# Optimization experiments

Hardware: AMD Instinct MI355X
Metric: run time of the kernel (lower is better)

## Reference

```python
import jax, jax.numpy as jnp
import numpy as np

T, A = 2048, 64          # n_thread, n_agents
RAWOB, N_TP, N_GP = 120, 5, 2
E = N_TP * N_GP          # number of sub-nets (type x group placeholder)
D = RAWOB + N_TP + 1     # augmented obs dim fed to each Net
H = 128                  # hidden width of each sub-net MLP
N_ACTION = 16


def setup_inputs() -> dict:
    key = jax.random.key(0)
    ks = jax.random.split(key, 12)
    s1 = 1.0 / np.sqrt(D)
    s2 = 1.0 / np.sqrt(H)
    return {
        "obs": jax.random.normal(ks[0], (T, A, RAWOB), dtype=jnp.float32),
        "hete_pick": jax.random.randint(ks[1], (T, A), 0, E),
        "hete_type": jax.random.randint(ks[2], (T, A), 0, N_TP),
        "gp_sel_summary": jax.random.randint(ks[3], (T, N_TP), 0, N_GP),
        # per-expert actor MLP params [E, ...]
        "W1": jax.random.normal(ks[4], (E, D, H), dtype=jnp.float32) * s1,
        "b1": jnp.zeros((E, H), dtype=jnp.float32),
        "W2": jax.random.normal(ks[5], (E, H, N_ACTION), dtype=jnp.float32) * s2,
        "b2": jnp.zeros((E, N_ACTION), dtype=jnp.float32),
        # central critic params
        "Wc1": jax.random.normal(ks[6], (D, H), dtype=jnp.float32) * s1,
        "bc1": jnp.zeros((H,), dtype=jnp.float32),
        "Wc2": jax.random.normal(ks[7], (H, 1), dtype=jnp.float32) * s2,
        "bc2": jnp.zeros((1,), dtype=jnp.float32),
    }


def _augment_obs(obs, hete_type, gp_sel_summary):
    # obs <- cat(obs, hete_type, gp_sel_summary with -1 scattered at own type idx)
    t, a, _ = obs.shape
    n_tp = gp_sel_summary.shape[1]
    gp = jnp.broadcast_to(gp_sel_summary[:, None, :].astype(obs.dtype), (t, a, n_tp))
    oh = jax.nn.one_hot(hete_type, n_tp, dtype=obs.dtype)
    gp_obs = gp * (1.0 - oh) - oh  # scatter -1 at index hete_type
    return jnp.concatenate([obs, hete_type[..., None].astype(obs.dtype), gp_obs], axis=-1)


def reference(obs, hete_pick, hete_type, gp_sel_summary,
              W1, b1, W2, b2, Wc1, bc1, Wc2, bc2):
    t, a, _ = obs.shape
    x = _augment_obs(obs, hete_type, gp_sel_summary)          # [T, A, D]
    xf = x.reshape(t * a, -1)                                  # [N, D]
    pick = hete_pick.reshape(t * a)                            # [N]
    n_exp = W1.shape[0]
    # dispatch: each token routed to exactly one sub-net; dense compute + masked combine
    logits = jnp.zeros((t * a, W2.shape[-1]), dtype=obs.dtype)
    for e in range(n_exp):  # small fixed expert loop
        y = jax.nn.relu(xf @ W1[e] + b1[e]) @ W2[e] + b2[e]    # [N, n_action]
        logits = jnp.where((pick == e)[:, None], y, logits)
    logits = logits.reshape(t, a, -1)
    # central critic on all tokens
    value = (jax.nn.relu(xf @ Wc1 + bc1) @ Wc2 + bc2).reshape(t, a, 1)
    return logits, value
```

## Files before the change

kernel.cpp:

```cpp
#include <hip/hip_runtime.h>
#include <hip/hip_bf16.h>

#define T_DIM   2048
#define A_DIM   64
#define N_TOK   (T_DIM * A_DIM)
#define RAWOB   120
#define N_TP    5
#define E_EXP   10
#define D_DIM   126
#define DP      128
#define H_DIM   128
#define N_ACT   16
#define CAP     16384
#define MTILE   64
#define MAXC    (CAP / MTILE)
#define LOGITS_SZ (N_TOK * N_ACT)
#define XS_STRIDE 136

typedef __bf16 bh8 __attribute__((ext_vector_type(8)));
typedef float  f32x4 __attribute__((ext_vector_type(4)));

__device__ __forceinline__ f32x4 mfma16(bh8 a, bh8 b, f32x4 c) {
    return __builtin_amdgcn_mfma_f32_16x16x32_bf16(a, b, c, 0, 0, 0);
}

__device__ __forceinline__ float bf2f(ushort u) {
    unsigned x = ((unsigned)u) << 16;
    return __builtin_bit_cast(float, x);
}
__device__ __forceinline__ ushort f2bf(float f) {
    unsigned x = __builtin_bit_cast(unsigned, f);
    unsigned r = (x + 0x7fffu + ((x >> 16) & 1u)) >> 16;
    return (ushort)r;
}

#define W1T_N (E_EXP * H_DIM * DP)
#define W2T_N (E_EXP * N_ACT * H_DIM)
#define WC1T_N (DP * DP)
#define PREP_BLOCKS 124

__global__ __launch_bounds__(256) void prep_kernel(
    const float* __restrict__ W1, const float* __restrict__ W2,
    const float* __restrict__ Wc1,
    int* __restrict__ counts, ushort* __restrict__ W1t,
    ushort* __restrict__ W2t, ushort* __restrict__ Wc1t)
{
    int bx = blockIdx.x, tid = threadIdx.x;
    if (bx < 44) {
        __shared__ ushort st[32][130];
        const float* src;
        ushort* dstbase;
        int d0;
        if (bx < 40) {
            int e = bx >> 2;
            d0 = (bx & 3) * 32;
            src = W1 + (e * D_DIM + d0) * H_DIM;
            dstbase = W1t + e * H_DIM * DP;
        } else {
            d0 = (bx - 40) * 32;
            src = Wc1 + d0 * H_DIM;
            dstbase = Wc1t;
        }
        int dmax = D_DIM - d0;
#pragma unroll
        for (int p = 0; p < 16; ++p) {
            int idx = p * 256 + tid;
            int dd = idx >> 7, h = idx & 127;
            float v = (dd < dmax) ? src[dd * H_DIM + h] : 0.f;
            st[dd][h] = f2bf(v);
        }
        __syncthreads();
#pragma unroll
        for (int p = 0; p < 16; ++p) {
            int idx = p * 256 + tid;
            int h = idx >> 5, d = idx & 31;
            dstbase[h * DP + d0 + d] = st[d][h];
        }
    } else {
        int i = (bx - 44) * 256 + tid;
        int h = i & 127;
        int a = (i >> 7) & 15;
        int e = i >> 11;
        W2t[(e * N_ACT + a) * H_DIM + h] = f2bf(W2[(e * H_DIM + h) * N_ACT + a]);
        if (bx == 44 && tid < 160) counts[tid] = 0;
    }
}

#define BUCKET_BLOCKS 128
__global__ __launch_bounds__(256) void bucket_kernel(
    const int* __restrict__ pick, int* __restrict__ counts, int* __restrict__ order)
{
    __shared__ int lc[E_EXP], lb[E_EXP], lcur[E_EXP];
    int tid = threadIdx.x;
    if (tid < E_EXP) { lc[tid] = 0; lcur[tid] = 0; }
    __syncthreads();
    int base = blockIdx.x * 1024;
    int e4[4];
#pragma unroll
    for (int it = 0; it < 4; ++it) {
        e4[it] = pick[base + it * 256 + tid];
        atomicAdd(&lc[e4[it]], 1);
    }
    __syncthreads();
    if (tid < E_EXP) lb[tid] = atomicAdd(&counts[tid * 16], lc[tid]);
    __syncthreads();
#pragma unroll
    for (int it = 0; it < 4; ++it) {
        int e = e4[it];
        int pos = lb[e] + atomicAdd(&lcur[e], 1);
        if (pos < CAP) order[e * CAP + pos] = base + it * 256 + tid;
    }
}

__device__ __forceinline__ void gemm64_relu(
    const ushort* xs, const ushort* __restrict__ Wt,
    const float* __restrict__ bias, ushort* hs, int w, int l)
{
    const int n0 = w * 32;
    const int lm = l & 15;
    const int lq = l >> 4;

    f32x4 acc[4][2];
#pragma unroll
    for (int mt = 0; mt < 4; ++mt) {
        acc[mt][0] = (f32x4){0.f, 0.f, 0.f, 0.f};
        acc[mt][1] = (f32x4){0.f, 0.f, 0.f, 0.f};
    }
    bh8 bfrag[4][2];
#pragma unroll
    for (int kt = 0; kt < 4; ++kt)
#pragma unroll
        for (int nt = 0; nt < 2; ++nt)
            bfrag[kt][nt] = *(const bh8*)(const void*)
                (Wt + (n0 + nt * 16 + lm) * DP + kt * 32 + lq * 8);

#pragma unroll
    for (int kt = 0; kt < 4; ++kt) {
#pragma unroll
        for (int mt = 0; mt < 4; ++mt) {
            bh8 a = *(const bh8*)(const void*)
                (xs + (mt * 16 + lm) * XS_STRIDE + kt * 32 + lq * 8);
            acc[mt][0] = mfma16(a, bfrag[kt][0], acc[mt][0]);
            acc[mt][1] = mfma16(a, bfrag[kt][1], acc[mt][1]);
        }
    }
    float bn0 = bias[n0 + lm];
    float bn1 = bias[n0 + 16 + lm];
#pragma unroll
    for (int mt = 0; mt < 4; ++mt) {
#pragma unroll
        for (int nt = 0; nt < 2; ++nt) {
            float bn = nt ? bn1 : bn0;
            int n = n0 + nt * 16 + lm;
#pragma unroll
            for (int r = 0; r < 4; ++r) {
                int m = mt * 16 + lq * 4 + r;
                float vf = acc[mt][nt][r] + bn;
                vf = fmaxf(vf, 0.f);
                hs[m * XS_STRIDE + n] = f2bf(vf);
            }
        }
    }
}

__global__ __launch_bounds__(256) void moe_kernel(
    const float* __restrict__ obs, const int* __restrict__ hete_type,
    const int* __restrict__ gp_sel,
    const float* __restrict__ b1, const float* __restrict__ b2,
    const float* __restrict__ bc1, const float* __restrict__ bc2,
    const int* __restrict__ counts, const int* __restrict__ order,
    const ushort* __restrict__ W1t, const ushort* __restrict__ W2t,
    const ushort* __restrict__ Wc1t, const float* __restrict__ Wc2,
    float* __restrict__ out)
{
    __shared__ int idx_s[MTILE];
    __shared__ __align__(16) ushort xs[MTILE * XS_STRIDE];
    __shared__ __align__(16) ushort hs[MTILE * XS_STRIDE];
    __shared__ float wc2s[128];

    const int bx = blockIdx.x;
    const int e = bx % E_EXP;
    const int c = bx / E_EXP;
    const int cnt = counts[e * 16];
    const int start = c * MTILE;
    if (start >= cnt) return;
    const int v = min(MTILE, cnt - start);

    const int tid = threadIdx.x;
    if (tid < MTILE) {
        int tok = 0;
        if (tid < v) tok = order[e * CAP + start + tid];
        idx_s[tid] = tok;
    } else if (tid < MTILE + 128) {
        wc2s[tid - MTILE] = Wc2[tid - MTILE];
    }
    __syncthreads();

    const int ck = (tid & 15) * 8;
    const int r0 = tid >> 4;
#pragma unroll
    for (int j = 0; j < 4; ++j) {
        int row = r0 + j * 16;
        int tok = idx_s[row];
        ushort* dst = &xs[row * XS_STRIDE + ck];
        if (ck < RAWOB) {
            const float* src = obs + tok * RAWOB + ck;
            float4 u0 = *(const float4*)(const void*)src;
            float4 u1 = *(const float4*)(const void*)(src + 4);
            dst[0] = f2bf(u0.x); dst[1] = f2bf(u0.y);
            dst[2] = f2bf(u0.z); dst[3] = f2bf(u0.w);
            dst[4] = f2bf(u1.x); dst[5] = f2bf(u1.y);
            dst[6] = f2bf(u1.z); dst[7] = f2bf(u1.w);
        } else {
            int ht = hete_type[tok];
            int tt = tok >> 6;
            dst[0] = f2bf((float)ht);
#pragma unroll
            for (int q = 0; q < N_TP; ++q) {
                float g = (q == ht) ? -1.0f : (float)gp_sel[tt * N_TP + q];
                dst[1 + q] = f2bf(g);
            }
            dst[6] = 0; dst[7] = 0;
        }
    }
    __syncthreads();

    const int w = tid >> 6;
    const int l = tid & 63;
    const int lm = l & 15;
    const int lq = l >> 4;

    gemm64_relu(xs, W1t + e * DP * DP, b1 + e * H_DIM, hs, w, l);
    __syncthreads();

    {
        f32x4 acc2 = (f32x4){0.f, 0.f, 0.f, 0.f};
        bh8 bfrag[4];
#pragma unroll
        for (int kt = 0; kt < 4; ++kt)
            bfrag[kt] = *(const bh8*)(const void*)
                (W2t + (e * N_ACT + lm) * H_DIM + kt * 32 + lq * 8);
#pragma unroll
        for (int kt = 0; kt < 4; ++kt) {
            bh8 a = *(const bh8*)(const void*)
                (hs + (w * 16 + lm) * XS_STRIDE + kt * 32 + lq * 8);
            acc2 = mfma16(a, bfrag[kt], acc2);
        }
        float bb = b2[e * N_ACT + lm];
#pragma unroll
        for (int r = 0; r < 4; ++r) {
            int m = w * 16 + lq * 4 + r;
            if (m < v) {
                int tok = idx_s[m];
                out[tok * N_ACT + lm] = acc2[r] + bb;
            }
        }
    }
    __syncthreads();

    gemm64_relu(xs, Wc1t, bc1, hs, w, l);
    __syncthreads();

    if (tid < 128) {
        int m = tid >> 1;
        int half = tid & 1;
        const ushort* hr = &hs[m * XS_STRIDE + half * 64];
        const float* wr = &wc2s[half * 64];
        float s = 0.f;
#pragma unroll
        for (int n = 0; n < 64; ++n) s += bf2f(hr[n]) * wr[n];
        float so = __shfl_xor(s, 1, 64);
        float vt = s + so + bc2[0];
        if (half == 0 && m < v) {
            out[LOGITS_SZ + idx_s[m]] = vt;
        }
    }
}

extern "C" void kernel_launch(void* const* d_in, const int* in_sizes, int n_in,
                              void* d_out, int out_size, void* d_ws, size_t ws_size,
                              hipStream_t stream) {
    const float* obs  = (const float*)d_in[0];
    const int*   pick = (const int*)d_in[1];
    const int*   htyp = (const int*)d_in[2];
    const int*   gp   = (const int*)d_in[3];
    const float* W1   = (const float*)d_in[4];
    const float* b1   = (const float*)d_in[5];
    const float* W2   = (const float*)d_in[6];
    const float* b2   = (const float*)d_in[7];
    const float* Wc1  = (const float*)d_in[8];
    const float* bc1  = (const float*)d_in[9];
    const float* Wc2  = (const float*)d_in[10];
    const float* bc2  = (const float*)d_in[11];
    float* out = (float*)d_out;

    int*    counts = (int*)d_ws;
    int*    order  = counts + 160;
    ushort* W1t    = (ushort*)(order + E_EXP * CAP);
    ushort* W2t    = W1t + W1T_N;
    ushort* Wc1t   = W2t + W2T_N;

    prep_kernel<<<PREP_BLOCKS, 256, 0, stream>>>(
        W1, W2, Wc1, counts, W1t, W2t, Wc1t);
    bucket_kernel<<<BUCKET_BLOCKS, 256, 0, stream>>>(pick, counts, order);
    moe_kernel<<<E_EXP * MAXC, 256, 0, stream>>>(
        obs, htyp, gp, b1, b2, bc1, bc2, counts, order,
        W1t, W2t, Wc1t, Wc2, out);
}
```

Baseline: 158.0 us.

## Halve token tile, fuse critic second layer into registers, raise occupancy

Shrinks the per-block token tile from 64 to 32 rows, which doubles the block count and halves shared memory per block, and adds a launch-bounds occupancy hint of 8 blocks. The critic's second layer (dot with Wc2) is now done in registers via shuffle reductions and a small cross-wave reduction buffer, instead of writing the hidden activations to shared memory and reading them back. This drops one barrier and the hs round trip. In exchange, weight fragments are reloaded per block more often, and only two waves do the actor output GEMM. The per-expert capacity constant is also reduced.

Measured after the change: 160.5 us. About the same (+1.6%).

```diff
diff --git a/kernel.cpp b/kernel.cpp
--- a/kernel.cpp
+++ b/kernel.cpp
@@ -11,8 +11,8 @@
 #define DP      128
 #define H_DIM   128
 #define N_ACT   16
-#define CAP     16384
-#define MTILE   64
+#define CAP     14336
+#define MTILE   32
 #define MAXC    (CAP / MTILE)
 #define LOGITS_SZ (N_TOK * N_ACT)
 #define XS_STRIDE 136
@@ -24,10 +24,6 @@
     return __builtin_amdgcn_mfma_f32_16x16x32_bf16(a, b, c, 0, 0, 0);
 }
 
-__device__ __forceinline__ float bf2f(ushort u) {
-    unsigned x = ((unsigned)u) << 16;
-    return __builtin_bit_cast(float, x);
-}
 __device__ __forceinline__ ushort f2bf(float f) {
     unsigned x = __builtin_bit_cast(unsigned, f);
     unsigned r = (x + 0x7fffu + ((x >> 16) & 1u)) >> 16;
@@ -112,58 +108,7 @@
     }
 }
 
-__device__ __forceinline__ void gemm64_relu(
-    const ushort* xs, const ushort* __restrict__ Wt,
-    const float* __restrict__ bias, ushort* hs, int w, int l)
-{
-    const int n0 = w * 32;
-    const int lm = l & 15;
-    const int lq = l >> 4;
-
-    f32x4 acc[4][2];
-#pragma unroll
-    for (int mt = 0; mt < 4; ++mt) {
-        acc[mt][0] = (f32x4){0.f, 0.f, 0.f, 0.f};
-        acc[mt][1] = (f32x4){0.f, 0.f, 0.f, 0.f};
-    }
-    bh8 bfrag[4][2];
-#pragma unroll
-    for (int kt = 0; kt < 4; ++kt)
-#pragma unroll
-        for (int nt = 0; nt < 2; ++nt)
-            bfrag[kt][nt] = *(const bh8*)(const void*)
-                (Wt + (n0 + nt * 16 + lm) * DP + kt * 32 + lq * 8);
-
-#pragma unroll
-    for (int kt = 0; kt < 4; ++kt) {
-#pragma unroll
-        for (int mt = 0; mt < 4; ++mt) {
-            bh8 a = *(const bh8*)(const void*)
-                (xs + (mt * 16 + lm) * XS_STRIDE + kt * 32 + lq * 8);
-            acc[mt][0] = mfma16(a, bfrag[kt][0], acc[mt][0]);
-            acc[mt][1] = mfma16(a, bfrag[kt][1], acc[mt][1]);
-        }
-    }
-    float bn0 = bias[n0 + lm];
-    float bn1 = bias[n0 + 16 + lm];
-#pragma unroll
-    for (int mt = 0; mt < 4; ++mt) {
-#pragma unroll
-        for (int nt = 0; nt < 2; ++nt) {
-            float bn = nt ? bn1 : bn0;
-            int n = n0 + nt * 16 + lm;
-#pragma unroll
-            for (int r = 0; r < 4; ++r) {
-                int m = mt * 16 + lq * 4 + r;
-                float vf = acc[mt][nt][r] + bn;
-                vf = fmaxf(vf, 0.f);
-                hs[m * XS_STRIDE + n] = f2bf(vf);
-            }
-        }
-    }
-}
-
-__global__ __launch_bounds__(256) void moe_kernel(
+__global__ __launch_bounds__(256, 8) void moe_kernel(
     const float* __restrict__ obs, const int* __restrict__ hete_type,
     const int* __restrict__ gp_sel,
     const float* __restrict__ b1, const float* __restrict__ b2,
@@ -176,7 +121,7 @@
     __shared__ int idx_s[MTILE];
     __shared__ __align__(16) ushort xs[MTILE * XS_STRIDE];
     __shared__ __align__(16) ushort hs[MTILE * XS_STRIDE];
-    __shared__ float wc2s[128];
+    __shared__ float red[4][MTILE];
 
     const int bx = blockIdx.x;
     const int e = bx % E_EXP;
@@ -191,15 +136,13 @@
         int tok = 0;
         if (tid < v) tok = order[e * CAP + start + tid];
         idx_s[tid] = tok;
-    } else if (tid < MTILE + 128) {
-        wc2s[tid - MTILE] = Wc2[tid - MTILE];
     }
     __syncthreads();
 
     const int ck = (tid & 15) * 8;
     const int r0 = tid >> 4;
 #pragma unroll
-    for (int j = 0; j < 4; ++j) {
+    for (int j = 0; j < 2; ++j) {
         int row = r0 + j * 16;
         int tok = idx_s[row];
         ushort* dst = &xs[row * XS_STRIDE + ck];
@@ -229,22 +172,55 @@
     const int l = tid & 63;
     const int lm = l & 15;
     const int lq = l >> 4;
-
-    gemm64_relu(xs, W1t + e * DP * DP, b1 + e * H_DIM, hs, w, l);
-    __syncthreads();
+    const int n0 = w * 32;
 
     {
+        const ushort* Wt = W1t + e * DP * DP;
+        f32x4 acc[2][2];
+#pragma unroll
+        for (int mt = 0; mt < 2; ++mt) {
+            acc[mt][0] = (f32x4){0.f, 0.f, 0.f, 0.f};
+            acc[mt][1] = (f32x4){0.f, 0.f, 0.f, 0.f};
+        }
+#pragma unroll
+        for (int kt = 0; kt < 4; ++kt) {
+            bh8 bf0 = *(const bh8*)(const void*)(Wt + (n0 + lm) * DP + kt * 32 + lq * 8);
+            bh8 bf1 = *(const bh8*)(const void*)(Wt + (n0 + 16 + lm) * DP + kt * 32 + lq * 8);
+#pragma unroll
+            for (int mt = 0; mt < 2; ++mt) {
+                bh8 a = *(const bh8*)(const void*)
+                    (xs + (mt * 16 + lm) * XS_STRIDE + kt * 32 + lq * 8);
+                acc[mt][0] = mfma16(a, bf0, acc[mt][0]);
+                acc[mt][1] = mfma16(a, bf1, acc[mt][1]);
+            }
+        }
+        float bn0 = b1[e * H_DIM + n0 + lm];
+        float bn1 = b1[e * H_DIM + n0 + 16 + lm];
+#pragma unroll
+        for (int mt = 0; mt < 2; ++mt)
+#pragma unroll
+            for (int nt = 0; nt < 2; ++nt) {
+                float bn = nt ? bn1 : bn0;
+                int n = n0 + nt * 16 + lm;
+#pragma unroll
+                for (int r = 0; r < 4; ++r) {
+                    int m = mt * 16 + lq * 4 + r;
+                    float vf = fmaxf(acc[mt][nt][r] + bn, 0.f);
+                    hs[m * XS_STRIDE + n] = f2bf(vf);
+                }
+            }
+    }
+    __syncthreads();
+
+    if (w < 2) {
         f32x4 acc2 = (f32x4){0.f, 0.f, 0.f, 0.f};
-        bh8 bfrag[4];
-#pragma unroll
-        for (int kt = 0; kt < 4; ++kt)
-            bfrag[kt] = *(const bh8*)(const void*)
+#pragma unroll
+        for (int kt = 0; kt < 4; ++kt) {
+            bh8 bf = *(const bh8*)(const void*)
                 (W2t + (e * N_ACT + lm) * H_DIM + kt * 32 + lq * 8);
-#pragma unroll
-        for (int kt = 0; kt < 4; ++kt) {
             bh8 a = *(const bh8*)(const void*)
                 (hs + (w * 16 + lm) * XS_STRIDE + kt * 32 + lq * 8);
-            acc2 = mfma16(a, bfrag[kt], acc2);
+            acc2 = mfma16(a, bf, acc2);
         }
         float bb = b2[e * N_ACT + lm];
 #pragma unroll
@@ -256,24 +232,55 @@
             }
         }
     }
-    __syncthreads();
-
-    gemm64_relu(xs, Wc1t, bc1, hs, w, l);
-    __syncthreads();
-
-    if (tid < 128) {
-        int m = tid >> 1;
-        int half = tid & 1;
-        const ushort* hr = &hs[m * XS_STRIDE + half * 64];
-        const float* wr = &wc2s[half * 64];
-        float s = 0.f;
-#pragma unroll
-        for (int n = 0; n < 64; ++n) s += bf2f(hr[n]) * wr[n];
-        float so = __shfl_xor(s, 1, 64);
-        float vt = s + so + bc2[0];
-        if (half == 0 && m < v) {
-            out[LOGITS_SZ + idx_s[m]] = vt;
-        }
+
+    {
+        f32x4 acc[2][2];
+#pragma unroll
+        for (int mt = 0; mt < 2; ++mt) {
+            acc[mt][0] = (f32x4){0.f, 0.f, 0.f, 0.f};
+            acc[mt][1] = (f32x4){0.f, 0.f, 0.f, 0.f};
+        }
+#pragma unroll
+        for (int kt = 0; kt < 4; ++kt) {
+            bh8 bf0 = *(const bh8*)(const void*)(Wc1t + (n0 + lm) * DP + kt * 32 + lq * 8);
+            bh8 bf1 = *(const bh8*)(const void*)(Wc1t + (n0 + 16 + lm) * DP + kt * 32 + lq * 8);
+#pragma unroll
+            for (int mt = 0; mt < 2; ++mt) {
+                bh8 a = *(const bh8*)(const void*)
+                    (xs + (mt * 16 + lm) * XS_STRIDE + kt * 32 + lq * 8);
+                acc[mt][0] = mfma16(a, bf0, acc[mt][0]);
+                acc[mt][1] = mfma16(a, bf1, acc[mt][1]);
+            }
+        }
+        float bn0 = bc1[n0 + lm],   wcv0 = Wc2[n0 + lm];
+        float bn1 = bc1[n0 + 16 + lm], wcv1 = Wc2[n0 + 16 + lm];
+        float part[2][4];
+#pragma unroll
+        for (int mt = 0; mt < 2; ++mt)
+#pragma unroll
+            for (int r = 0; r < 4; ++r)
+                part[mt][r] = fmaxf(acc[mt][0][r] + bn0, 0.f) * wcv0
+                            + fmaxf(acc[mt][1][r] + bn1, 0.f) * wcv1;
+#pragma unroll
+        for (int mask = 1; mask < 16; mask <<= 1)
+#pragma unroll
+            for (int mt = 0; mt < 2; ++mt)
+#pragma unroll
+                for (int r = 0; r < 4; ++r)
+                    part[mt][r] += __shfl_xor(part[mt][r], mask, 64);
+        if (lm == 0) {
+#pragma unroll
+            for (int mt = 0; mt < 2; ++mt)
+#pragma unroll
+                for (int r = 0; r < 4; ++r)
+                    red[w][mt * 16 + lq * 4 + r] = part[mt][r];
+        }
+    }
+    __syncthreads();
+
+    if (tid < MTILE && tid < v) {
+        float vt = red[0][tid] + red[1][tid] + red[2][tid] + red[3][tid] + bc2[0];
+        out[LOGITS_SZ + idx_s[tid]] = vt;
     }
 }
 
```

## Restructure MoE kernel so each wave owns 16 tokens with register-resident A fragments

Applied to the files above, without the earlier changes.

Each wave now gathers its own 16 tokens straight from global memory into MFMA A-fragments in registers, instead of the whole block staging a 64-row shared tile. The expert and critic first-layer GEMMs are fused into one loop that shares the A fragments. The critic head is reduced in registers with shuffles, which removes its shared-memory pass and all block-level barriers. Each wave now streams the full W1/Wc1 B operands from global/L2 itself rather than splitting N across waves, so weight traffic per token rises. CAP is lowered, occupancy is hinted via launch bounds, and shared memory shrinks to a per-wave hidden buffer.

Result: slower. 192.0 us (+21.6%).

```diff
diff --git a/kernel.cpp b/kernel.cpp
--- a/kernel.cpp
+++ b/kernel.cpp
@@ -11,23 +11,20 @@
 #define DP      128
 #define H_DIM   128
 #define N_ACT   16
-#define CAP     16384
+#define CAP     14336
 #define MTILE   64
 #define MAXC    (CAP / MTILE)
 #define LOGITS_SZ (N_TOK * N_ACT)
-#define XS_STRIDE 136
+#define HB_STRIDE 136
 
 typedef __bf16 bh8 __attribute__((ext_vector_type(8)));
+typedef ushort u16x8 __attribute__((ext_vector_type(8)));
 typedef float  f32x4 __attribute__((ext_vector_type(4)));
 
 __device__ __forceinline__ f32x4 mfma16(bh8 a, bh8 b, f32x4 c) {
     return __builtin_amdgcn_mfma_f32_16x16x32_bf16(a, b, c, 0, 0, 0);
 }
 
-__device__ __forceinline__ float bf2f(ushort u) {
-    unsigned x = ((unsigned)u) << 16;
-    return __builtin_bit_cast(float, x);
-}
 __device__ __forceinline__ ushort f2bf(float f) {
     unsigned x = __builtin_bit_cast(unsigned, f);
     unsigned r = (x + 0x7fffu + ((x >> 16) & 1u)) >> 16;
@@ -112,58 +109,7 @@
     }
 }
 
-__device__ __forceinline__ void gemm64_relu(
-    const ushort* xs, const ushort* __restrict__ Wt,
-    const float* __restrict__ bias, ushort* hs, int w, int l)
-{
-    const int n0 = w * 32;
-    const int lm = l & 15;
-    const int lq = l >> 4;
-
-    f32x4 acc[4][2];
-#pragma unroll
-    for (int mt = 0; mt < 4; ++mt) {
-        acc[mt][0] = (f32x4){0.f, 0.f, 0.f, 0.f};
-        acc[mt][1] = (f32x4){0.f, 0.f, 0.f, 0.f};
-    }
-    bh8 bfrag[4][2];
-#pragma unroll
-    for (int kt = 0; kt < 4; ++kt)
-#pragma unroll
-        for (int nt = 0; nt < 2; ++nt)
-            bfrag[kt][nt] = *(const bh8*)(const void*)
-                (Wt + (n0 + nt * 16 + lm) * DP + kt * 32 + lq * 8);
-
-#pragma unroll
-    for (int kt = 0; kt < 4; ++kt) {
-#pragma unroll
-        for (int mt = 0; mt < 4; ++mt) {
-            bh8 a = *(const bh8*)(const void*)
-                (xs + (mt * 16 + lm) * XS_STRIDE + kt * 32 + lq * 8);
-            acc[mt][0] = mfma16(a, bfrag[kt][0], acc[mt][0]);
-            acc[mt][1] = mfma16(a, bfrag[kt][1], acc[mt][1]);
-        }
-    }
-    float bn0 = bias[n0 + lm];
-    float bn1 = bias[n0 + 16 + lm];
-#pragma unroll
-    for (int mt = 0; mt < 4; ++mt) {
-#pragma unroll
-        for (int nt = 0; nt < 2; ++nt) {
-            float bn = nt ? bn1 : bn0;
-            int n = n0 + nt * 16 + lm;
-#pragma unroll
-            for (int r = 0; r < 4; ++r) {
-                int m = mt * 16 + lq * 4 + r;
-                float vf = acc[mt][nt][r] + bn;
-                vf = fmaxf(vf, 0.f);
-                hs[m * XS_STRIDE + n] = f2bf(vf);
-            }
-        }
-    }
-}
-
-__global__ __launch_bounds__(256) void moe_kernel(
+__global__ __launch_bounds__(256, 6) void moe_kernel(
     const float* __restrict__ obs, const int* __restrict__ hete_type,
     const int* __restrict__ gp_sel,
     const float* __restrict__ b1, const float* __restrict__ b2,
@@ -173,106 +119,118 @@
     const ushort* __restrict__ Wc1t, const float* __restrict__ Wc2,
     float* __restrict__ out)
 {
-    __shared__ int idx_s[MTILE];
-    __shared__ __align__(16) ushort xs[MTILE * XS_STRIDE];
-    __shared__ __align__(16) ushort hs[MTILE * XS_STRIDE];
-    __shared__ float wc2s[128];
+    __shared__ __align__(16) ushort hbuf[4][16 * HB_STRIDE];
 
     const int bx = blockIdx.x;
     const int e = bx % E_EXP;
     const int c = bx / E_EXP;
     const int cnt = counts[e * 16];
-    const int start = c * MTILE;
-    if (start >= cnt) return;
-    const int v = min(MTILE, cnt - start);
-
     const int tid = threadIdx.x;
-    if (tid < MTILE) {
-        int tok = 0;
-        if (tid < v) tok = order[e * CAP + start + tid];
-        idx_s[tid] = tok;
-    } else if (tid < MTILE + 128) {
-        wc2s[tid - MTILE] = Wc2[tid - MTILE];
-    }
-    __syncthreads();
-
-    const int ck = (tid & 15) * 8;
-    const int r0 = tid >> 4;
-#pragma unroll
-    for (int j = 0; j < 4; ++j) {
-        int row = r0 + j * 16;
-        int tok = idx_s[row];
-        ushort* dst = &xs[row * XS_STRIDE + ck];
-        if (ck < RAWOB) {
-            const float* src = obs + tok * RAWOB + ck;
-            float4 u0 = *(const float4*)(const void*)src;
-            float4 u1 = *(const float4*)(const void*)(src + 4);
-            dst[0] = f2bf(u0.x); dst[1] = f2bf(u0.y);
-            dst[2] = f2bf(u0.z); dst[3] = f2bf(u0.w);
-            dst[4] = f2bf(u1.x); dst[5] = f2bf(u1.y);
-            dst[6] = f2bf(u1.z); dst[7] = f2bf(u1.w);
+    const int w = tid >> 6;
+    const int base = c * MTILE + w * 16;
+    if (base >= cnt) return;
+
+    const int l = tid & 63;
+    const int lm = l & 15;
+    const int lq = l >> 4;
+
+    const int slot = min(base + lm, cnt - 1);
+    const int tok = order[e * CAP + slot];
+
+    bh8 a[4];
+    {
+        const float* orow = obs + tok * RAWOB;
+#pragma unroll
+        for (int kt = 0; kt < 3; ++kt) {
+            const float* p = orow + kt * 32 + lq * 8;
+            float4 u0 = *(const float4*)(const void*)p;
+            float4 u1 = *(const float4*)(const void*)(p + 4);
+            u16x8 t;
+            t[0] = f2bf(u0.x); t[1] = f2bf(u0.y); t[2] = f2bf(u0.z); t[3] = f2bf(u0.w);
+            t[4] = f2bf(u1.x); t[5] = f2bf(u1.y); t[6] = f2bf(u1.z); t[7] = f2bf(u1.w);
+            a[kt] = __builtin_bit_cast(bh8, t);
+        }
+        u16x8 t;
+        if (lq < 3) {
+            const float* p = orow + 96 + lq * 8;
+            float4 u0 = *(const float4*)(const void*)p;
+            float4 u1 = *(const float4*)(const void*)(p + 4);
+            t[0] = f2bf(u0.x); t[1] = f2bf(u0.y); t[2] = f2bf(u0.z); t[3] = f2bf(u0.w);
+            t[4] = f2bf(u1.x); t[5] = f2bf(u1.y); t[6] = f2bf(u1.z); t[7] = f2bf(u1.w);
         } else {
             int ht = hete_type[tok];
             int tt = tok >> 6;
-            dst[0] = f2bf((float)ht);
+            t[0] = f2bf((float)ht);
 #pragma unroll
             for (int q = 0; q < N_TP; ++q) {
                 float g = (q == ht) ? -1.0f : (float)gp_sel[tt * N_TP + q];
-                dst[1 + q] = f2bf(g);
+                t[1 + q] = f2bf(g);
             }
-            dst[6] = 0; dst[7] = 0;
-        }
-    }
-    __syncthreads();
-
-    const int w = tid >> 6;
-    const int l = tid & 63;
-    const int lm = l & 15;
-    const int lq = l >> 4;
-
-    gemm64_relu(xs, W1t + e * DP * DP, b1 + e * H_DIM, hs, w, l);
-    __syncthreads();
+            t[6] = 0; t[7] = 0;
+        }
+        a[3] = __builtin_bit_cast(bh8, t);
+    }
+
+    ushort* hrow = &hbuf[w][0];
+    const ushort* W1e = W1t + e * DP * DP;
+    float part[4] = {0.f, 0.f, 0.f, 0.f};
+#pragma unroll
+    for (int nt = 0; nt < 8; ++nt) {
+        const int n = nt * 16 + lm;
+        f32x4 ae = (f32x4){0.f, 0.f, 0.f, 0.f};
+        f32x4 ac = (f32x4){0.f, 0.f, 0.f, 0.f};
+#pragma unroll
+        for (int kt = 0; kt < 4; ++kt) {
+            bh8 be = *(const bh8*)(const void*)(W1e + n * DP + kt * 32 + lq * 8);
+            bh8 bc = *(const bh8*)(const void*)(Wc1t + n * DP + kt * 32 + lq * 8);
+            ae = mfma16(a[kt], be, ae);
+            ac = mfma16(a[kt], bc, ac);
+        }
+        float bn = b1[e * H_DIM + n];
+        float cn = bc1[n];
+        float wc = Wc2[n];
+#pragma unroll
+        for (int r = 0; r < 4; ++r) {
+            float hv = fmaxf(ae[r] + bn, 0.f);
+            hrow[(lq * 4 + r) * HB_STRIDE + n] = f2bf(hv);
+            part[r] += fmaxf(ac[r] + cn, 0.f) * wc;
+        }
+    }
+
+#pragma unroll
+    for (int mask = 1; mask < 16; mask <<= 1)
+#pragma unroll
+        for (int r = 0; r < 4; ++r)
+            part[r] += __shfl_xor(part[r], mask, 64);
+    if (lm == 0) {
+        float bcv = bc2[0];
+#pragma unroll
+        for (int r = 0; r < 4; ++r) {
+            int m = lq * 4 + r;
+            if (base + m < cnt) {
+                int tm = order[e * CAP + base + m];
+                out[LOGITS_SZ + tm] = part[r] + bcv;
+            }
+        }
+    }
 
     {
-        f32x4 acc2 = (f32x4){0.f, 0.f, 0.f, 0.f};
-        bh8 bfrag[4];
-#pragma unroll
-        for (int kt = 0; kt < 4; ++kt)
-            bfrag[kt] = *(const bh8*)(const void*)
+        f32x4 y = (f32x4){0.f, 0.f, 0.f, 0.f};
+#pragma unroll
+        for (int kt = 0; kt < 4; ++kt) {
+            bh8 hf = *(const bh8*)(const void*)(hrow + lm * HB_STRIDE + kt * 32 + lq * 8);
+            bh8 bf = *(const bh8*)(const void*)
                 (W2t + (e * N_ACT + lm) * H_DIM + kt * 32 + lq * 8);
-#pragma unroll
-        for (int kt = 0; kt < 4; ++kt) {
-            bh8 a = *(const bh8*)(const void*)
-                (hs + (w * 16 + lm) * XS_STRIDE + kt * 32 + lq * 8);
-            acc2 = mfma16(a, bfrag[kt], acc2);
+            y = mfma16(hf, bf, y);
         }
         float bb = b2[e * N_ACT + lm];
 #pragma unroll
         for (int r = 0; r < 4; ++r) {
-            int m = w * 16 + lq * 4 + r;
-            if (m < v) {
-                int tok = idx_s[m];
-                out[tok * N_ACT + lm] = acc2[r] + bb;
+            int m = lq * 4 + r;
+            if (base + m < cnt) {
+                int tm = order[e * CAP + base + m];
+                out[tm * N_ACT + lm] = y[r] + bb;
             }
-        }
-    }
-    __syncthreads();
-
-    gemm64_relu(xs, Wc1t, bc1, hs, w, l);
-    __syncthreads();
-
-    if (tid < 128) {
-        int m = tid >> 1;
-        int half = tid & 1;
-        const ushort* hr = &hs[m * XS_STRIDE + half * 64];
-        const float* wr = &wc2s[half * 64];
-        float s = 0.f;
-#pragma unroll
-        for (int n = 0; n < 64; ++n) s += bf2f(hr[n]) * wr[n];
-        float so = __shfl_xor(s, 1, 64);
-        float vt = s + so + bc2[0];
-        if (half == 0 && m < v) {
-            out[LOGITS_SZ + idx_s[m]] = vt;
         }
     }
 }
```
